# Optimization experiments

Measured on AMD Instinct MI355X. Metric: run time of the kernel, lower is better.

## Reference

```python
import jax, jax.numpy as jnp
import numpy as np

ALPHA = 0.2          # LeakyReLU negative slope
NEG_INF = -9e15      # mask value used by the original module
B, L, D, F_IN, F_OUT = 16, 256, 128, 64, 64


def setup_inputs() -> dict:
    key = jax.random.key(0)
    k1, k2, k3, k4 = jax.random.split(key, 4)
    h = jax.random.normal(k1, (B, L, D, F_IN), dtype=jnp.float32)
    adj = jax.random.randint(k2, (B, L, D, D), 0, 2, dtype=jnp.int32)
    # xavier_uniform(gain=1.414) bounds
    bW = 1.414 * np.sqrt(6.0 / (F_IN + F_OUT))
    W = jax.random.uniform(k3, (F_IN, F_OUT), dtype=jnp.float32, minval=-bW, maxval=bW)
    ba = 1.414 * np.sqrt(6.0 / (2 * F_OUT + 1))
    a = jax.random.uniform(k4, (2 * F_OUT, 1), dtype=jnp.float32, minval=-ba, maxval=ba)
    return {"h": h, "adj": adj, "W": W, "a": a}


def reference(h, adj, W, a):
    # h: [B,L,D,F_in], adj: [B,L,D,D]
    Wh = jnp.einsum('bldf,fo->bldo', h, W)              # [B,L,D,F_out]
    a1 = a[:F_OUT, 0]                                    # dots the "source" node i
    a2 = a[F_OUT:, 0]                                    # dots the "target" node j
    e_i = Wh @ a1                                        # [B,L,D]
    e_j = Wh @ a2                                        # [B,L,D]
    e = e_i[..., :, None] + e_j[..., None, :]            # [B,L,D,D] pairwise scores
    e = jnp.where(e > 0, e, ALPHA * e)                   # LeakyReLU
    att = jnp.where(adj > 0, e, NEG_INF)
    att = jax.nn.softmax(att, axis=-1)                   # dropout=eval mode (no-op)
    h_prime = jnp.einsum('bldk,blko->bldo', att, Wh)     # [B,L,D,F_out]
    return h_prime
```

## Files before the change

kernel.cpp:

```cpp
#include <hip/hip_runtime.h>

constexpr int D_   = 128;
constexpr int FIN  = 64;
constexpr int FOUT = 64;
constexpr float ALPHA = 0.2f;

typedef _Float16 f16x8 __attribute__((ext_vector_type(8)));
typedef float    f32x4 __attribute__((ext_vector_type(4)));

__global__ __launch_bounds__(256, 4) void gat_kernel(
    const float* __restrict__ hg, const int* __restrict__ adjg,
    const float* __restrict__ Wg, const float* __restrict__ ag,
    float* __restrict__ outg)
{
    __shared__ __align__(16) unsigned short sX[128 * 64];
    __shared__ __align__(16) unsigned short sPt[64 * 64];
    __shared__ __align__(16) float sA[2 * FOUT];
    __shared__ float sEi[D_];
    __shared__ __align__(16) float sEj[D_];
    __shared__ float sL[D_];
    __shared__ float sMxW[4];

    const int tid  = threadIdx.x;
    const int lane = tid & 63;
    const int w    = tid >> 6;
    const int g    = lane >> 4;
    const int m16  = lane & 15;

    const long bl = blockIdx.x;
    const float* hp   = hg   + bl * (long)(D_ * FIN);
    const int*   adjp = adjg + bl * (long)(D_ * D_);
    float*       outp = outg + bl * (long)(D_ * FOUT);

    char* xb = (char*)sX;
    char* pb = (char*)sPt;

    const int pi  = tid >> 1;
    const int pjb = (tid & 1) << 4;

    {
        const float4* h4 = (const float4*)hp;
        #pragma unroll
        for (int k = 0; k < 8; ++k) {
            int idx = tid + 256 * k;
            float4 v = h4[idx];
            int row = idx >> 4;
            int f   = (idx & 15) << 2;
            union { _Float16 h[4]; uint2 u; } cv;
            cv.h[0] = (_Float16)v.x; cv.h[1] = (_Float16)v.y;
            cv.h[2] = (_Float16)v.z; cv.h[3] = (_Float16)v.w;
            int off = (row * 128 + f * 2) ^ ((row & 7) << 4);
            *(uint2*)(xb + off) = cv.u;
        }
        {
            const int f0 = (tid & 15) * 4;
            const int o0 = (tid >> 4) * 4;
            float4 r0 = *(const float4*)&Wg[(f0 + 0) * 64 + o0];
            float4 r1 = *(const float4*)&Wg[(f0 + 1) * 64 + o0];
            float4 r2 = *(const float4*)&Wg[(f0 + 2) * 64 + o0];
            float4 r3 = *(const float4*)&Wg[(f0 + 3) * 64 + o0];
            float col[4][4] = {{r0.x, r1.x, r2.x, r3.x},
                               {r0.y, r1.y, r2.y, r3.y},
                               {r0.z, r1.z, r2.z, r3.z},
                               {r0.w, r1.w, r2.w, r3.w}};
            #pragma unroll
            for (int c = 0; c < 4; ++c) {
                int o = o0 + c;
                union { _Float16 h[4]; uint2 u; } cv;
                cv.h[0] = (_Float16)col[c][0]; cv.h[1] = (_Float16)col[c][1];
                cv.h[2] = (_Float16)col[c][2]; cv.h[3] = (_Float16)col[c][3];
                int off = (o * 128 + f0 * 2) ^ ((o & 7) << 4);
                *(uint2*)(pb + off) = cv.u;
            }
        }
        if (tid < 2 * FOUT) sA[tid] = ag[tid];
    }

    int4 areg[4];
    {
        const int4* ap = (const int4*)(adjp + pi * D_ + pjb);
        #pragma unroll
        for (int q = 0; q < 4; ++q) areg[q] = ap[q];
    }
    __syncthreads();

    f32x4 acc[2][4];
    #pragma unroll
    for (int mt = 0; mt < 2; ++mt)
        #pragma unroll
        for (int nt = 0; nt < 4; ++nt) acc[mt][nt] = (f32x4){0.f, 0.f, 0.f, 0.f};

    #pragma unroll
    for (int kt = 0; kt < 2; ++kt) {
        f16x8 af[2], bf[4];
        #pragma unroll
        for (int mt = 0; mt < 2; ++mt) {
            int row = w * 32 + mt * 16 + m16;
            af[mt] = *(const f16x8*)(xb + ((row * 128 + kt * 64 + g * 16) ^ ((row & 7) << 4)));
        }
        #pragma unroll
        for (int nt = 0; nt < 4; ++nt) {
            int o = nt * 16 + m16;
            bf[nt] = *(const f16x8*)(pb + ((o * 128 + kt * 64 + g * 16) ^ ((o & 7) << 4)));
        }
        #pragma unroll
        for (int mt = 0; mt < 2; ++mt)
            #pragma unroll
            for (int nt = 0; nt < 4; ++nt)
                acc[mt][nt] = __builtin_amdgcn_mfma_f32_16x16x32_f16(af[mt], bf[nt], acc[mt][nt], 0, 0, 0);
    }
    __syncthreads();

    {
        float a1v[4], a2v[4];
        #pragma unroll
        for (int nt = 0; nt < 4; ++nt) {
            a1v[nt] = sA[nt * 16 + m16];
            a2v[nt] = sA[FOUT + nt * 16 + m16];
        }
        float wmax = -3.0e38f;
        #pragma unroll
        for (int mt = 0; mt < 2; ++mt) {
            #pragma unroll
            for (int r = 0; r < 4; ++r) {
                float ei = 0.f, ej = 0.f;
                #pragma unroll
                for (int nt = 0; nt < 4; ++nt) {
                    float v = acc[mt][nt][r];
                    ei += v * a1v[nt];
                    ej += v * a2v[nt];
                }
                #pragma unroll
                for (int s = 1; s < 16; s <<= 1) {
                    ei += __shfl_xor(ei, s);
                    ej += __shfl_xor(ej, s);
                }
                int row = w * 32 + mt * 16 + g * 4 + r;
                if (m16 == 0) { sEi[row] = ei; sEj[row] = ej; }
                wmax = fmaxf(wmax, ej);
            }
        }
        wmax = fmaxf(wmax, __shfl_xor(wmax, 16));
        wmax = fmaxf(wmax, __shfl_xor(wmax, 32));
        if (lane == 0) sMxW[w] = wmax;

        #pragma unroll
        for (int mt = 0; mt < 2; ++mt) {
            int j0r = w * 32 + mt * 16 + g * 4;
            #pragma unroll
            for (int nt = 0; nt < 4; ++nt) {
                int o = nt * 16 + m16;
                union { _Float16 h[4]; uint2 u; } cv;
                cv.h[0] = (_Float16)acc[mt][nt][0];
                cv.h[1] = (_Float16)acc[mt][nt][1];
                cv.h[2] = (_Float16)acc[mt][nt][2];
                cv.h[3] = (_Float16)acc[mt][nt][3];
                int off = (o * 256 + j0r * 2) ^ ((o & 7) << 4);
                *(uint2*)(xb + off) = cv.u;
            }
        }
    }
    __syncthreads();

    #pragma unroll
    for (int mt = 0; mt < 2; ++mt)
        #pragma unroll
        for (int nt = 0; nt < 4; ++nt) acc[mt][nt] = (f32x4){0.f, 0.f, 0.f, 0.f};

    const float ei_pi = sEi[pi];
    const float mxj = fmaxf(fmaxf(sMxW[0], sMxW[1]), fmaxf(sMxW[2], sMxW[3]));
    float mt_ = ei_pi + mxj;
    const float mi = mt_ > 0.f ? mt_ : ALPHA * mt_;
    float lpt = 0.f;

    #pragma unroll
    for (int jt = 0; jt < 4; ++jt) {
        const int j0 = jt * 32;
        union { _Float16 h[8]; uint4 u; } ph0, ph1;
        #pragma unroll
        for (int q = 0; q < 4; ++q) {
            int4 av = areg[q];
            int aa[4] = {av.x, av.y, av.z, av.w};
            float4 ej4 = *(const float4*)&sEj[j0 + pjb + q * 4];
            float ejv[4] = {ej4.x, ej4.y, ej4.z, ej4.w};
            #pragma unroll
            for (int kk = 0; kk < 4; ++kk) {
                float e = ei_pi + ejv[kk];
                e = e > 0.f ? e : ALPHA * e;
                float p = (aa[kk] > 0) ? __expf(e - mi) : 0.f;
                lpt += p;
                _Float16 pv = (_Float16)p;
                if (q < 2) ph0.h[q * 4 + kk] = pv;
                else       ph1.h[(q - 2) * 4 + kk] = pv;
            }
        }
        {
            int base = pi * 64 + pjb * 2;
            *(uint4*)(pb + ((base)      ^ ((pi & 3) << 4))) = ph0.u;
            *(uint4*)(pb + ((base + 16) ^ ((pi & 3) << 4))) = ph1.u;
        }
        if (jt < 3) {
            const int4* ap = (const int4*)(adjp + pi * D_ + (jt + 1) * 32 + pjb);
            #pragma unroll
            for (int q = 0; q < 4; ++q) areg[q] = ap[q];
        }

        f16x8 pa[2], wb[4];
        #pragma unroll
        for (int mtx = 0; mtx < 2; ++mtx) {
            int i = w * 32 + mtx * 16 + m16;
            pa[mtx] = *(const f16x8*)(pb + ((i * 64 + g * 16) ^ ((i & 3) << 4)));
        }
        #pragma unroll
        for (int nt = 0; nt < 4; ++nt) {
            int o = nt * 16 + m16;
            wb[nt] = *(const f16x8*)(xb + ((o * 256 + j0 * 2 + g * 16) ^ ((o & 7) << 4)));
        }
        #pragma unroll
        for (int mtx = 0; mtx < 2; ++mtx)
            #pragma unroll
            for (int nt = 0; nt < 4; ++nt)
                acc[mtx][nt] = __builtin_amdgcn_mfma_f32_16x16x32_f16(pa[mtx], wb[nt], acc[mtx][nt], 0, 0, 0);
    }

    lpt += __shfl_xor(lpt, 1);
    if ((tid & 1) == 0) sL[pi] = lpt;

    #pragma unroll
    for (int mtx = 0; mtx < 2; ++mtx) {
        #pragma unroll
        for (int r = 0; r < 4; ++r) {
            int row = w * 32 + mtx * 16 + g * 4 + r;
            float inv = 1.0f / sL[row];
            #pragma unroll
            for (int nt = 0; nt < 4; ++nt)
                outp[row * 64 + nt * 16 + m16] = acc[mtx][nt][r] * inv;
        }
    }
}

extern "C" void kernel_launch(void* const* d_in, const int* in_sizes, int n_in,
                              void* d_out, int out_size, void* d_ws, size_t ws_size,
                              hipStream_t stream) {
    const float* h   = (const float*)d_in[0];
    const int*   adj = (const int*)d_in[1];
    const float* W   = (const float*)d_in[2];
    const float* a   = (const float*)d_in[3];
    float*       out = (float*)d_out;
    gat_kernel<<<dim3(16 * 256), dim3(256), 0, stream>>>(h, adj, W, a, out);
}
```

Measured before the change: 475.4 us.

## Compute attention probabilities directly in MFMA A-fragment layout, skipping LDS staging

Each lane now computes the softmax numerators for exactly the rows and columns it needs as MFMA A-operand fragments, instead of computing a row-pair tile and writing it to shared memory for a reread. This removes the LDS store/load round trip for P in every j-tile. The adjacency loads are remapped to match: each lane reads two 8-int segments from two rows. Row sums are now reduced with cross-group shuffles. The trade-off is less coalesced global reads of adj, because lanes now stride across rows.

```diff
diff --git a/kernel.cpp b/kernel.cpp
--- a/kernel.cpp
+++ b/kernel.cpp
@@ -35,9 +35,6 @@
     char* xb = (char*)sX;
     char* pb = (char*)sPt;
 
-    const int pi  = tid >> 1;
-    const int pjb = (tid & 1) << 4;
-
     {
         const float4* h4 = (const float4*)hp;
         #pragma unroll
@@ -76,12 +73,14 @@
         if (tid < 2 * FOUT) sA[tid] = ag[tid];
     }
 
+    const int row0 = w * 32 + m16;
+    const int* aprow0 = adjp + row0 * D_ + g * 8;
+    const int* aprow1 = aprow0 + 16 * D_;
     int4 areg[4];
-    {
-        const int4* ap = (const int4*)(adjp + pi * D_ + pjb);
-        #pragma unroll
-        for (int q = 0; q < 4; ++q) areg[q] = ap[q];
-    }
+    areg[0] = *(const int4*)(aprow0);
+    areg[1] = *(const int4*)(aprow0 + 4);
+    areg[2] = *(const int4*)(aprow1);
+    areg[3] = *(const int4*)(aprow1 + 4);
     __syncthreads();
 
     f32x4 acc[2][4];
@@ -167,64 +166,66 @@
         #pragma unroll
         for (int nt = 0; nt < 4; ++nt) acc[mt][nt] = (f32x4){0.f, 0.f, 0.f, 0.f};
 
-    const float ei_pi = sEi[pi];
+    const float ei0 = sEi[row0];
+    const float ei1 = sEi[row0 + 16];
     const float mxj = fmaxf(fmaxf(sMxW[0], sMxW[1]), fmaxf(sMxW[2], sMxW[3]));
-    float mt_ = ei_pi + mxj;
-    const float mi = mt_ > 0.f ? mt_ : ALPHA * mt_;
-    float lpt = 0.f;
+    float t0 = ei0 + mxj, t1 = ei1 + mxj;
+    const float mi0 = t0 > 0.f ? t0 : ALPHA * t0;
+    const float mi1 = t1 > 0.f ? t1 : ALPHA * t1;
+    float lp0 = 0.f, lp1 = 0.f;
 
     #pragma unroll
     for (int jt = 0; jt < 4; ++jt) {
         const int j0 = jt * 32;
-        union { _Float16 h[8]; uint4 u; } ph0, ph1;
-        #pragma unroll
-        for (int q = 0; q < 4; ++q) {
-            int4 av = areg[q];
-            int aa[4] = {av.x, av.y, av.z, av.w};
-            float4 ej4 = *(const float4*)&sEj[j0 + pjb + q * 4];
-            float ejv[4] = {ej4.x, ej4.y, ej4.z, ej4.w};
-            #pragma unroll
-            for (int kk = 0; kk < 4; ++kk) {
-                float e = ei_pi + ejv[kk];
-                e = e > 0.f ? e : ALPHA * e;
-                float p = (aa[kk] > 0) ? __expf(e - mi) : 0.f;
-                lpt += p;
-                _Float16 pv = (_Float16)p;
-                if (q < 2) ph0.h[q * 4 + kk] = pv;
-                else       ph1.h[(q - 2) * 4 + kk] = pv;
-            }
-        }
-        {
-            int base = pi * 64 + pjb * 2;
-            *(uint4*)(pb + ((base)      ^ ((pi & 3) << 4))) = ph0.u;
-            *(uint4*)(pb + ((base + 16) ^ ((pi & 3) << 4))) = ph1.u;
+        float4 ejA = *(const float4*)&sEj[j0 + g * 8];
+        float4 ejB = *(const float4*)&sEj[j0 + g * 8 + 4];
+        float ejv[8] = {ejA.x, ejA.y, ejA.z, ejA.w, ejB.x, ejB.y, ejB.z, ejB.w};
+        int aa0[8] = {areg[0].x, areg[0].y, areg[0].z, areg[0].w,
+                      areg[1].x, areg[1].y, areg[1].z, areg[1].w};
+        int aa1[8] = {areg[2].x, areg[2].y, areg[2].z, areg[2].w,
+                      areg[3].x, areg[3].y, areg[3].z, areg[3].w};
+        f16x8 pa0, pa1;
+        #pragma unroll
+        for (int q = 0; q < 8; ++q) {
+            float e0 = ei0 + ejv[q];
+            e0 = e0 > 0.f ? e0 : ALPHA * e0;
+            float p0 = (aa0[q] > 0) ? __expf(e0 - mi0) : 0.f;
+            lp0 += p0;
+            pa0[q] = (_Float16)p0;
+            float e1 = ei1 + ejv[q];
+            e1 = e1 > 0.f ? e1 : ALPHA * e1;
+            float p1 = (aa1[q] > 0) ? __expf(e1 - mi1) : 0.f;
+            lp1 += p1;
+            pa1[q] = (_Float16)p1;
         }
         if (jt < 3) {
-            const int4* ap = (const int4*)(adjp + pi * D_ + (jt + 1) * 32 + pjb);
-            #pragma unroll
-            for (int q = 0; q < 4; ++q) areg[q] = ap[q];
-        }
-
-        f16x8 pa[2], wb[4];
-        #pragma unroll
-        for (int mtx = 0; mtx < 2; ++mtx) {
-            int i = w * 32 + mtx * 16 + m16;
-            pa[mtx] = *(const f16x8*)(pb + ((i * 64 + g * 16) ^ ((i & 3) << 4)));
-        }
+            const int* n0 = aprow0 + (jt + 1) * 32;
+            const int* n1 = aprow1 + (jt + 1) * 32;
+            areg[0] = *(const int4*)(n0);
+            areg[1] = *(const int4*)(n0 + 4);
+            areg[2] = *(const int4*)(n1);
+            areg[3] = *(const int4*)(n1 + 4);
+        }
+
+        f16x8 wb[4];
         #pragma unroll
         for (int nt = 0; nt < 4; ++nt) {
             int o = nt * 16 + m16;
             wb[nt] = *(const f16x8*)(xb + ((o * 256 + j0 * 2 + g * 16) ^ ((o & 7) << 4)));
         }
         #pragma unroll
-        for (int mtx = 0; mtx < 2; ++mtx)
-            #pragma unroll
-            for (int nt = 0; nt < 4; ++nt)
-                acc[mtx][nt] = __builtin_amdgcn_mfma_f32_16x16x32_f16(pa[mtx], wb[nt], acc[mtx][nt], 0, 0, 0);
-    }
-
-    lpt += __shfl_xor(lpt, 1);
-    if ((tid & 1) == 0) sL[pi] = lpt;
+        for (int nt = 0; nt < 4; ++nt) {
+            acc[0][nt] = __builtin_amdgcn_mfma_f32_16x16x32_f16(pa0, wb[nt], acc[0][nt], 0, 0, 0);
+            acc[1][nt] = __builtin_amdgcn_mfma_f32_16x16x32_f16(pa1, wb[nt], acc[1][nt], 0, 0, 0);
+        }
+    }
+
+    lp0 += __shfl_xor(lp0, 16); lp0 += __shfl_xor(lp0, 32);
+    lp1 += __shfl_xor(lp1, 16); lp1 += __shfl_xor(lp1, 32);
+    if (g == 0) {
+        sL[row0]      = lp0;
+        sL[row0 + 16] = lp1;
+    }
 
     #pragma unroll
     for (int mtx = 0; mtx < 2; ++mtx) {
```

Result: no change. 476.0 us (+0.1%).
